# Kernel optimization log

Measured on AMD Instinct MI355X. Metric: run time of the kernel, lower is better.

## Reference

```python
import jax, jax.numpy as jnp
import numpy as np

N_NODES = 50000
N_EDGES = 640000
IN_FEAT = 128
H_FEAT = 128
OUT_FEAT = 128
N_CLASSES = 16
BN_EPS = 1e-5


def gcn_conv(x, W, b, edge_index, n_nodes):
    """PyG GCNConv: add self-loops, symmetric deg^{-1/2} normalization,
    gather -> weighted message -> scatter_add, plus bias."""
    loop = jnp.arange(n_nodes, dtype=edge_index.dtype)
    src = jnp.concatenate([edge_index[0], loop])  # [E+N]
    dst = jnp.concatenate([edge_index[1], loop])  # [E+N]
    ones = jnp.ones(src.shape[0], dtype=x.dtype)
    deg = jax.ops.segment_sum(ones, dst, num_segments=n_nodes)  # >=1 (self loops)
    dinv = jax.lax.rsqrt(deg)
    norm = dinv[src] * dinv[dst]  # [E+N]
    h = x @ W  # [N, F_out]
    msgs = h[src] * norm[:, None]  # gather + scale, [E+N, F_out]
    out = jax.ops.segment_sum(msgs, dst, num_segments=n_nodes)  # scatter_add
    return out + b


def setup_inputs() -> dict:
    key = jax.random.key(0)
    ks = jax.random.split(key, 10)
    seq = jax.random.normal(ks[0], (N_NODES, IN_FEAT), dtype=jnp.float32)
    edge_index = jax.random.randint(ks[1], (2, N_EDGES), 0, N_NODES, dtype=jnp.int64)
    s1 = 1.0 / np.sqrt(IN_FEAT)
    s2 = 1.0 / np.sqrt(H_FEAT)
    s3 = 1.0 / np.sqrt(OUT_FEAT)
    W1 = jax.random.uniform(ks[2], (IN_FEAT, H_FEAT), jnp.float32, -s1, s1)
    b1 = jnp.zeros((H_FEAT,), jnp.float32)
    gamma = jnp.ones((H_FEAT,), jnp.float32)
    beta = jnp.zeros((H_FEAT,), jnp.float32)
    running_mean = 0.1 * jax.random.normal(ks[3], (H_FEAT,), jnp.float32)
    running_var = jax.random.uniform(ks[4], (H_FEAT,), jnp.float32, 0.5, 1.5)
    W2 = jax.random.uniform(ks[5], (H_FEAT, OUT_FEAT), jnp.float32, -s2, s2)
    b2 = jnp.zeros((OUT_FEAT,), jnp.float32)
    Wc = jax.random.uniform(ks[6], (OUT_FEAT, N_CLASSES), jnp.float32, -s3, s3)
    bc = jax.random.uniform(ks[7], (N_CLASSES,), jnp.float32, -s3, s3)
    return {
        "seq": seq, "edge_index": edge_index,
        "W1": W1, "b1": b1, "gamma": gamma, "beta": beta,
        "running_mean": running_mean, "running_var": running_var,
        "W2": W2, "b2": b2, "Wc": Wc, "bc": bc,
    }


def reference(seq, edge_index, W1, b1, gamma, beta, running_mean, running_var, W2, b2, Wc, bc):
    # inference mode: BN uses running stats, dropout is identity
    n = seq.shape[0]
    h = gcn_conv(seq, W1, b1, edge_index, n)
    h = (h - running_mean) * jax.lax.rsqrt(running_var + BN_EPS) * gamma + beta
    h = jax.nn.relu(h)
    h = gcn_conv(h, W2, b2, edge_index, n)
    return h @ Wc + bc
```

## Files before the change

kernel.cpp:

```cpp
#include <hip/hip_runtime.h>
#include <math.h>

#define N_NODES 50000
#define N_EDGES 640000
#define FDIM 128
#define NCLS 16
#define BN_EPS 1e-5f
#define NBS 196
#define NBG 782

typedef __attribute__((ext_vector_type(8))) short bf16x8;
typedef __attribute__((ext_vector_type(4))) float f32x4;

__device__ __forceinline__ unsigned pack_bf16x2(float lo, float hi) {
    unsigned ul = __float_as_uint(lo);
    unsigned uh = __float_as_uint(hi);
    ul += 0x7fff + ((ul >> 16) & 1);
    uh += 0x7fff + ((uh >> 16) & 1);
    return (ul >> 16) | (uh & 0xffff0000u);
}
__device__ __forceinline__ unsigned short bf16_rne(float x) {
    unsigned u = __float_as_uint(x);
    u += 0x7fff + ((u >> 16) & 1);
    return (unsigned short)(u >> 16);
}
__device__ __forceinline__ float bf_lo(unsigned u) { return __uint_as_float(u << 16); }
__device__ __forceinline__ float bf_hi(unsigned u) { return __uint_as_float(u & 0xffff0000u); }

__global__ __launch_bounds__(256) void gemm_count_fold_kernel(
        const float* __restrict__ seq, const float* __restrict__ W1,
        unsigned* __restrict__ bufA,
        const int* __restrict__ eidx, int* __restrict__ deg,
        const float* __restrict__ W2, const float* __restrict__ Wc,
        const float* __restrict__ b1, const float* __restrict__ b2,
        const float* __restrict__ bc, const float* __restrict__ gamma,
        const float* __restrict__ beta, const float* __restrict__ rmean,
        const float* __restrict__ rvar,
        float* __restrict__ W2c, float* __restrict__ bc2, float4* __restrict__ fusedq) {
    __shared__ __align__(16) char smem[65536];
    int tid = threadIdx.x;
    int bid = blockIdx.x;

    if (bid < NBG) {
        bf16x8* WH = (bf16x8*)smem;
        bf16x8* WL = (bf16x8*)(smem + 32768);
        {
            int f0 = tid * 8;
#pragma unroll
            for (int fo = 0; fo < 8; fo++) {
                int fi = f0 + fo;
                int lane = fi & 63, kt = (fi >> 6) & 3, ct = fi >> 8;
                int kbase = kt * 32 + (lane >> 4) * 8;
                int col = ct * 16 + (lane & 15);
                short h[8], lo[8];
#pragma unroll
                for (int j = 0; j < 8; j++) {
                    float wv = W1[(kbase + j) * 128 + col];
                    unsigned short hs = bf16_rne(wv);
                    float rem = wv - __uint_as_float(((unsigned)hs) << 16);
                    h[j] = (short)hs;
                    lo[j] = (short)bf16_rne(rem);
                }
                WH[fi] = *(bf16x8*)h;
                WL[fi] = *(bf16x8*)lo;
            }
        }
        __syncthreads();

        int w = tid >> 6, l = tid & 63;
        int la = l & 15, q = l >> 4;
        int r0 = bid * 64;
        int arow = r0 + w * 16 + la;
        bool rowok = arow < N_NODES;
        const float4* X4 = (const float4*)seq;

        float4 xr[8];
#pragma unroll
        for (int kt = 0; kt < 4; kt++) {
            float4 z4 = make_float4(0.f, 0.f, 0.f, 0.f);
            xr[kt * 2]     = rowok ? X4[arow * 32 + kt * 8 + q * 2]     : z4;
            xr[kt * 2 + 1] = rowok ? X4[arow * 32 + kt * 8 + q * 2 + 1] : z4;
        }
        bf16x8 ah[4], al[4];
#pragma unroll
        for (int kt = 0; kt < 4; kt++) {
            const float* xv = (const float*)&xr[kt * 2];
#pragma unroll
            for (int j = 0; j < 8; j++) {
                float v = xv[j];
                unsigned short hs = bf16_rne(v);
                float rem = v - __uint_as_float(((unsigned)hs) << 16);
                ah[kt][j] = (short)hs;
                al[kt][j] = (short)bf16_rne(rem);
            }
        }
        f32x4 acc[8];
#pragma unroll
        for (int ct = 0; ct < 8; ct++) acc[ct] = (f32x4){0.f, 0.f, 0.f, 0.f};

#pragma unroll
        for (int kt = 0; kt < 4; kt++) {
#pragma unroll
            for (int ct = 0; ct < 8; ct++) {
                bf16x8 bh = WH[(ct * 4 + kt) * 64 + l];
                bf16x8 bl = WL[(ct * 4 + kt) * 64 + l];
                acc[ct] = __builtin_amdgcn_mfma_f32_16x16x32_bf16(ah[kt], bh, acc[ct], 0, 0, 0);
                acc[ct] = __builtin_amdgcn_mfma_f32_16x16x32_bf16(ah[kt], bl, acc[ct], 0, 0, 0);
                acc[ct] = __builtin_amdgcn_mfma_f32_16x16x32_bf16(al[kt], bh, acc[ct], 0, 0, 0);
            }
        }
        __syncthreads();

        float* sC = (float*)smem;
#pragma unroll
        for (int ct = 0; ct < 8; ct++)
#pragma unroll
            for (int r = 0; r < 4; r++)
                sC[(w * 16 + q * 4 + r) * 132 + ct * 16 + la] = acc[ct][r];
        __syncthreads();

        int trow = tid >> 2, tcb = (tid & 3) * 32;
        int grow = r0 + trow;
        if (grow < N_NODES) {
            const float* sr = sC + trow * 132 + tcb;
            unsigned ob[16];
#pragma unroll
            for (int t = 0; t < 16; t++) ob[t] = pack_bf16x2(sr[2 * t], sr[2 * t + 1]);
            uint4* dp = (uint4*)(bufA + (size_t)grow * 64 + (tid & 3) * 16);
#pragma unroll
            for (int g = 0; g < 4; g++)
                dp[g] = make_uint4(ob[g * 4], ob[g * 4 + 1], ob[g * 4 + 2], ob[g * 4 + 3]);
        }
    } else if (bid < NBG + 625) {
        const int4* dst4 = (const int4*)(eidx + N_EDGES);
        int t = (bid - NBG) * 256 + tid;
        int4 d = dst4[t];
        atomicAdd(&deg[d.x], 1);
        atomicAdd(&deg[d.y], 1);
        atomicAdd(&deg[d.z], 1);
        atomicAdd(&deg[d.w], 1);
    } else {
        int fb = bid - (NBG + 625);
        int gid = fb * 256 + tid;
        int r = gid >> 4, c = gid & 15;
        float acc = 0.f;
#pragma unroll 8
        for (int k = 0; k < 128; k++) acc += W2[r * 128 + k] * Wc[k * 16 + c];
        W2c[gid] = acc;
        if (fb == 0) {
            if (tid < 16) {
                float a = bc[tid];
                for (int k = 0; k < 128; k++) a += b2[k] * Wc[k * 16 + tid];
                bc2[tid] = a;
            }
            if (tid < 64) {
                int c0 = tid * 2, c1 = c0 + 1;
                float sc0 = gamma[c0] * rsqrtf(rvar[c0] + BN_EPS);
                float sc1 = gamma[c1] * rsqrtf(rvar[c1] + BN_EPS);
                float sh0 = (b1[c0] - rmean[c0]) * sc0 + beta[c0];
                float sh1 = (b1[c1] - rmean[c1]) * sc1 + beta[c1];
                fusedq[tid] = make_float4(sc0, sh0, sc1, sh1);
            }
        }
    }
}

__global__ __launch_bounds__(256) void scan_kernel(const int* __restrict__ deg,
                                                   int* __restrict__ offs,
                                                   int* __restrict__ partials,
                                                   float* __restrict__ dinv,
                                                   int* __restrict__ cursor,
                                                   int* __restrict__ done) {
    __shared__ int s[256];
    __shared__ int isLast;
    int tid = threadIdx.x;
    int gid = blockIdx.x * 256 + tid;
    int v = (gid < N_NODES) ? deg[gid] : 0;
    if (gid < N_NODES) {
        dinv[gid] = rsqrtf((float)(v + 1));
        cursor[gid] = 0;
    }
    s[tid] = v;
    __syncthreads();
    for (int off = 1; off < 256; off <<= 1) {
        int t2 = (tid >= off) ? s[tid - off] : 0;
        __syncthreads();
        s[tid] += t2;
        __syncthreads();
    }
    if (gid <= N_NODES) offs[gid] = s[tid] - v;
    if (tid == 255) partials[blockIdx.x] = s[255];

    __threadfence();
    if (tid == 0) isLast = (atomicAdd(done, 1) == NBS - 1);
    __syncthreads();
    if (isLast) {
        __threadfence();
        int pv = (tid < NBS) ? partials[tid] : 0;
        s[tid] = pv;
        __syncthreads();
        for (int off = 1; off < 256; off <<= 1) {
            int t2 = (tid >= off) ? s[tid - off] : 0;
            __syncthreads();
            s[tid] += t2;
            __syncthreads();
        }
        if (tid < NBS) partials[tid] = s[tid] - pv;
    }
}

__global__ __launch_bounds__(256) void fill_csr_kernel(const int* __restrict__ eidx,
                                                       const int* __restrict__ offs,
                                                       const int* __restrict__ part,
                                                       const float* __restrict__ dinv,
                                                       int* __restrict__ cursor,
                                                       int2* __restrict__ csr_sw) {
    const int4* src4 = (const int4*)eidx;
    const int4* dst4 = (const int4*)(eidx + N_EDGES);
    int t = blockIdx.x * 256 + threadIdx.x;
    int4 sv = src4[t];
    int4 dv = dst4[t];
    {
        int pos = offs[dv.x] + part[dv.x >> 8] + atomicAdd(&cursor[dv.x], 1);
        csr_sw[pos] = make_int2(sv.x, __float_as_int(dinv[sv.x]));
    }
    {
        int pos = offs[dv.y] + part[dv.y >> 8] + atomicAdd(&cursor[dv.y], 1);
        csr_sw[pos] = make_int2(sv.y, __float_as_int(dinv[sv.y]));
    }
    {
        int pos = offs[dv.z] + part[dv.z >> 8] + atomicAdd(&cursor[dv.z], 1);
        csr_sw[pos] = make_int2(sv.z, __float_as_int(dinv[sv.z]));
    }
    {
        int pos = offs[dv.w] + part[dv.w >> 8] + atomicAdd(&cursor[dv.w], 1);
        csr_sw[pos] = make_int2(sv.w, __float_as_int(dinv[sv.w]));
    }
}

__global__ __launch_bounds__(256) void agg1_kernel(const unsigned* __restrict__ Hb,
                                                   const int2* __restrict__ csr_sw,
                                                   const int* __restrict__ offs,
                                                   const int* __restrict__ part,
                                                   const float* __restrict__ dinv,
                                                   const float4* __restrict__ fusedq,
                                                   const float* __restrict__ W2c,
                                                   float* __restrict__ Z) {
    __shared__ float sH[4][128];
    int w = threadIdx.x >> 6, l = threadIdx.x & 63;
    int node = blockIdx.x * 4 + w;
    int beg = __builtin_amdgcn_readfirstlane(offs[node] + part[node >> 8]);
    int end = __builtin_amdgcn_readfirstlane(offs[node + 1] + part[(node + 1) >> 8]);
    float di = dinv[node];

    int c = l & 15, q = l >> 4;
    float wreg[32];
#pragma unroll
    for (int i = 0; i < 32; i++) wreg[i] = W2c[(q * 32 + i) * 16 + c];

    unsigned hv = Hb[(size_t)node * 64 + l];
    float n2 = di * di;
    float acc0 = bf_lo(hv) * n2, acc1 = bf_hi(hv) * n2;

    int e = beg;
    for (; e + 8 <= end; e += 8) {
        int2 a0 = csr_sw[e];     int2 a1 = csr_sw[e + 1];
        int2 a2 = csr_sw[e + 2]; int2 a3 = csr_sw[e + 3];
        int2 a4 = csr_sw[e + 4]; int2 a5 = csr_sw[e + 5];
        int2 a6 = csr_sw[e + 6]; int2 a7 = csr_sw[e + 7];
        unsigned u0 = Hb[(size_t)a0.x * 64 + l];
        unsigned u1 = Hb[(size_t)a1.x * 64 + l];
        unsigned u2 = Hb[(size_t)a2.x * 64 + l];
        unsigned u3 = Hb[(size_t)a3.x * 64 + l];
        unsigned u4 = Hb[(size_t)a4.x * 64 + l];
        unsigned u5 = Hb[(size_t)a5.x * 64 + l];
        unsigned u6 = Hb[(size_t)a6.x * 64 + l];
        unsigned u7 = Hb[(size_t)a7.x * 64 + l];
        float w0 = __int_as_float(a0.y) * di, w1 = __int_as_float(a1.y) * di;
        float w2 = __int_as_float(a2.y) * di, w3 = __int_as_float(a3.y) * di;
        float w4 = __int_as_float(a4.y) * di, w5 = __int_as_float(a5.y) * di;
        float w6 = __int_as_float(a6.y) * di, w7 = __int_as_float(a7.y) * di;
        acc0 += bf_lo(u0) * w0 + bf_lo(u1) * w1 + bf_lo(u2) * w2 + bf_lo(u3) * w3
              + bf_lo(u4) * w4 + bf_lo(u5) * w5 + bf_lo(u6) * w6 + bf_lo(u7) * w7;
        acc1 += bf_hi(u0) * w0 + bf_hi(u1) * w1 + bf_hi(u2) * w2 + bf_hi(u3) * w3
              + bf_hi(u4) * w4 + bf_hi(u5) * w5 + bf_hi(u6) * w6 + bf_hi(u7) * w7;
    }
    while (e < end) {
        int i1 = e + 1 < end ? e + 1 : end - 1;
        int i2 = e + 2 < end ? e + 2 : end - 1;
        int i3 = e + 3 < end ? e + 3 : end - 1;
        int2 a0 = csr_sw[e];  int2 a1 = csr_sw[i1];
        int2 a2 = csr_sw[i2]; int2 a3 = csr_sw[i3];
        unsigned u0 = Hb[(size_t)a0.x * 64 + l];
        unsigned u1 = Hb[(size_t)a1.x * 64 + l];
        unsigned u2 = Hb[(size_t)a2.x * 64 + l];
        unsigned u3 = Hb[(size_t)a3.x * 64 + l];
        float w0 = __int_as_float(a0.y) * di;
        float w1 = (e + 1 < end) ? __int_as_float(a1.y) * di : 0.f;
        float w2 = (e + 2 < end) ? __int_as_float(a2.y) * di : 0.f;
        float w3 = (e + 3 < end) ? __int_as_float(a3.y) * di : 0.f;
        acc0 += bf_lo(u0) * w0 + bf_lo(u1) * w1 + bf_lo(u2) * w2 + bf_lo(u3) * w3;
        acc1 += bf_hi(u0) * w0 + bf_hi(u1) * w1 + bf_hi(u2) * w2 + bf_hi(u3) * w3;
        e += 4;
    }

    float4 qv = fusedq[l];
    float a0 = fmaxf(acc0 * qv.x + qv.y, 0.f);
    float a1 = fmaxf(acc1 * qv.z + qv.w, 0.f);

    ((float2*)sH[w])[l] = make_float2(a0, a1);
    float z = 0.f;
    const float4* row4 = (const float4*)&sH[w][q * 32];
#pragma unroll
    for (int i = 0; i < 8; i++) {
        float4 v = row4[i];
        z += v.x * wreg[i * 4] + v.y * wreg[i * 4 + 1]
           + v.z * wreg[i * 4 + 2] + v.w * wreg[i * 4 + 3];
    }
    z += __shfl_xor(z, 16);
    z += __shfl_xor(z, 32);
    if (l < 16) Z[(size_t)node * NCLS + l] = z;
}

__global__ __launch_bounds__(256) void agg2_kernel(const float* __restrict__ Z,
                                                   const int2* __restrict__ csr_sw,
                                                   const int* __restrict__ offs,
                                                   const int* __restrict__ part,
                                                   const float* __restrict__ dinv,
                                                   const float* __restrict__ bc2,
                                                   float* __restrict__ out) {
    int grp = threadIdx.x >> 4, c = threadIdx.x & 15;
    int node = blockIdx.x * 16 + grp;
    int beg = offs[node] + part[node >> 8];
    int end = offs[node + 1] + part[(node + 1) >> 8];
    float di = dinv[node];

    float acc = Z[(size_t)node * NCLS + c] * di * di;
    int e = beg;
    for (; e + 8 <= end; e += 8) {
        int2 a0 = csr_sw[e],     a1 = csr_sw[e + 1];
        int2 a2 = csr_sw[e + 2], a3 = csr_sw[e + 3];
        int2 a4 = csr_sw[e + 4], a5 = csr_sw[e + 5];
        int2 a6 = csr_sw[e + 6], a7 = csr_sw[e + 7];
        float v0 = Z[(size_t)a0.x * NCLS + c];
        float v1 = Z[(size_t)a1.x * NCLS + c];
        float v2 = Z[(size_t)a2.x * NCLS + c];
        float v3 = Z[(size_t)a3.x * NCLS + c];
        float v4 = Z[(size_t)a4.x * NCLS + c];
        float v5 = Z[(size_t)a5.x * NCLS + c];
        float v6 = Z[(size_t)a6.x * NCLS + c];
        float v7 = Z[(size_t)a7.x * NCLS + c];
        acc += v0 * (__int_as_float(a0.y) * di) + v1 * (__int_as_float(a1.y) * di)
             + v2 * (__int_as_float(a2.y) * di) + v3 * (__int_as_float(a3.y) * di)
             + v4 * (__int_as_float(a4.y) * di) + v5 * (__int_as_float(a5.y) * di)
             + v6 * (__int_as_float(a6.y) * di) + v7 * (__int_as_float(a7.y) * di);
    }
    for (; e < end; e++) {
        int2 a = csr_sw[e];
        acc += Z[(size_t)a.x * NCLS + c] * (__int_as_float(a.y) * di);
    }
    out[(size_t)node * NCLS + c] = acc + bc2[c];
}

extern "C" void kernel_launch(void* const* d_in, const int* in_sizes, int n_in,
                              void* d_out, int out_size, void* d_ws, size_t ws_size,
                              hipStream_t stream) {
    const float* seq   = (const float*)d_in[0];
    const int*   eidx  = (const int*)d_in[1];
    const float* W1    = (const float*)d_in[2];
    const float* b1    = (const float*)d_in[3];
    const float* gamma = (const float*)d_in[4];
    const float* beta  = (const float*)d_in[5];
    const float* rmean = (const float*)d_in[6];
    const float* rvar  = (const float*)d_in[7];
    const float* W2    = (const float*)d_in[8];
    const float* b2    = (const float*)d_in[9];
    const float* Wc    = (const float*)d_in[10];
    const float* bc    = (const float*)d_in[11];

    char* ws = (char*)d_ws;
    size_t off = 0;
    auto alloc = [&](size_t bytes) -> void* {
        void* p = ws + off;
        off = (off + bytes + 255) & ~(size_t)255;
        return p;
    };
    int*    ctl      = (int*)alloc(256);
    int*    deg      = (int*)alloc(N_NODES * 4);
    int*    cursor   = (int*)alloc(N_NODES * 4);
    int*    offs     = (int*)alloc((N_NODES + 1) * 4);
    int*    partials = (int*)alloc(256 * 4);
    float*  dinv     = (float*)alloc(N_NODES * 4);
    int2*   csr_sw   = (int2*)alloc((size_t)N_EDGES * 8);
    float*  W2c      = (float*)alloc(FDIM * NCLS * 4);
    float*  bc2      = (float*)alloc(NCLS * 4);
    float4* fusedq   = (float4*)alloc(64 * 16);
    unsigned* bufA   = (unsigned*)alloc((size_t)N_NODES * (FDIM / 2) * 4);
    float*  Zbuf     = (float*)alloc((size_t)N_NODES * NCLS * 4);

    hipMemsetAsync(ctl, 0, 256 + (size_t)N_NODES * 4, stream);
    gemm_count_fold_kernel<<<NBG + 625 + 8, 256, 0, stream>>>(
        seq, W1, bufA, eidx, deg, W2, Wc, b1, b2, bc, gamma, beta, rmean, rvar,
        W2c, bc2, fusedq);
    scan_kernel<<<NBS, 256, 0, stream>>>(deg, offs, partials, dinv, cursor, ctl);
    fill_csr_kernel<<<625, 256, 0, stream>>>(eidx, offs, partials, dinv, cursor, csr_sw);
    agg1_kernel<<<N_NODES / 4, 256, 0, stream>>>(bufA, csr_sw, offs, partials,
                                                 dinv, fusedq, W2c, Zbuf);
    agg2_kernel<<<N_NODES / 16, 256, 0, stream>>>(Zbuf, csr_sw, offs, partials,
                                                  dinv, bc2, (float*)d_out);
}
```

Before: 229.2 us.

## Pre-pack W1 split-bf16 fragments once in a separate kernel, read from global in GEMM

Before, each of the 782 GEMM blocks rebuilt the full hi/lo bf16 split of W1 in 64KB of shared memory. That work now happens once in a small 16-block kernel that writes the fragments to global memory, and the GEMM blocks read B fragments straight from global/L2. The GEMM kernel's shared memory shrinks to the 33KB output staging tile, which could allow more resident blocks, and the staging readback is vectorised to float4. The cost is an extra kernel launch and serialisation, plus MFMA operands now coming from L2 instead of LDS.

Measured after the change: 234.4 us. +2.3%, slower.

```diff
diff --git a/kernel.cpp b/kernel.cpp
--- a/kernel.cpp
+++ b/kernel.cpp
@@ -27,127 +27,25 @@
 __device__ __forceinline__ float bf_lo(unsigned u) { return __uint_as_float(u << 16); }
 __device__ __forceinline__ float bf_hi(unsigned u) { return __uint_as_float(u & 0xffff0000u); }
 
-__global__ __launch_bounds__(256) void gemm_count_fold_kernel(
-        const float* __restrict__ seq, const float* __restrict__ W1,
-        unsigned* __restrict__ bufA,
-        const int* __restrict__ eidx, int* __restrict__ deg,
+__global__ __launch_bounds__(256) void packw_fold_kernel(
+        const float* __restrict__ W1,
         const float* __restrict__ W2, const float* __restrict__ Wc,
         const float* __restrict__ b1, const float* __restrict__ b2,
         const float* __restrict__ bc, const float* __restrict__ gamma,
         const float* __restrict__ beta, const float* __restrict__ rmean,
         const float* __restrict__ rvar,
+        bf16x8* __restrict__ WHg, bf16x8* __restrict__ WLg,
         float* __restrict__ W2c, float* __restrict__ bc2, float4* __restrict__ fusedq) {
-    __shared__ __align__(16) char smem[65536];
     int tid = threadIdx.x;
     int bid = blockIdx.x;
-
-    if (bid < NBG) {
-        bf16x8* WH = (bf16x8*)smem;
-        bf16x8* WL = (bf16x8*)(smem + 32768);
-        {
-            int f0 = tid * 8;
-#pragma unroll
-            for (int fo = 0; fo < 8; fo++) {
-                int fi = f0 + fo;
-                int lane = fi & 63, kt = (fi >> 6) & 3, ct = fi >> 8;
-                int kbase = kt * 32 + (lane >> 4) * 8;
-                int col = ct * 16 + (lane & 15);
-                short h[8], lo[8];
-#pragma unroll
-                for (int j = 0; j < 8; j++) {
-                    float wv = W1[(kbase + j) * 128 + col];
-                    unsigned short hs = bf16_rne(wv);
-                    float rem = wv - __uint_as_float(((unsigned)hs) << 16);
-                    h[j] = (short)hs;
-                    lo[j] = (short)bf16_rne(rem);
-                }
-                WH[fi] = *(bf16x8*)h;
-                WL[fi] = *(bf16x8*)lo;
-            }
-        }
-        __syncthreads();
-
-        int w = tid >> 6, l = tid & 63;
-        int la = l & 15, q = l >> 4;
-        int r0 = bid * 64;
-        int arow = r0 + w * 16 + la;
-        bool rowok = arow < N_NODES;
-        const float4* X4 = (const float4*)seq;
-
-        float4 xr[8];
-#pragma unroll
-        for (int kt = 0; kt < 4; kt++) {
-            float4 z4 = make_float4(0.f, 0.f, 0.f, 0.f);
-            xr[kt * 2]     = rowok ? X4[arow * 32 + kt * 8 + q * 2]     : z4;
-            xr[kt * 2 + 1] = rowok ? X4[arow * 32 + kt * 8 + q * 2 + 1] : z4;
-        }
-        bf16x8 ah[4], al[4];
-#pragma unroll
-        for (int kt = 0; kt < 4; kt++) {
-            const float* xv = (const float*)&xr[kt * 2];
-#pragma unroll
-            for (int j = 0; j < 8; j++) {
-                float v = xv[j];
-                unsigned short hs = bf16_rne(v);
-                float rem = v - __uint_as_float(((unsigned)hs) << 16);
-                ah[kt][j] = (short)hs;
-                al[kt][j] = (short)bf16_rne(rem);
-            }
-        }
-        f32x4 acc[8];
-#pragma unroll
-        for (int ct = 0; ct < 8; ct++) acc[ct] = (f32x4){0.f, 0.f, 0.f, 0.f};
-
-#pragma unroll
-        for (int kt = 0; kt < 4; kt++) {
-#pragma unroll
-            for (int ct = 0; ct < 8; ct++) {
-                bf16x8 bh = WH[(ct * 4 + kt) * 64 + l];
-                bf16x8 bl = WL[(ct * 4 + kt) * 64 + l];
-                acc[ct] = __builtin_amdgcn_mfma_f32_16x16x32_bf16(ah[kt], bh, acc[ct], 0, 0, 0);
-                acc[ct] = __builtin_amdgcn_mfma_f32_16x16x32_bf16(ah[kt], bl, acc[ct], 0, 0, 0);
-                acc[ct] = __builtin_amdgcn_mfma_f32_16x16x32_bf16(al[kt], bh, acc[ct], 0, 0, 0);
-            }
-        }
-        __syncthreads();
-
-        float* sC = (float*)smem;
-#pragma unroll
-        for (int ct = 0; ct < 8; ct++)
-#pragma unroll
-            for (int r = 0; r < 4; r++)
-                sC[(w * 16 + q * 4 + r) * 132 + ct * 16 + la] = acc[ct][r];
-        __syncthreads();
-
-        int trow = tid >> 2, tcb = (tid & 3) * 32;
-        int grow = r0 + trow;
-        if (grow < N_NODES) {
-            const float* sr = sC + trow * 132 + tcb;
-            unsigned ob[16];
-#pragma unroll
-            for (int t = 0; t < 16; t++) ob[t] = pack_bf16x2(sr[2 * t], sr[2 * t + 1]);
-            uint4* dp = (uint4*)(bufA + (size_t)grow * 64 + (tid & 3) * 16);
-#pragma unroll
-            for (int g = 0; g < 4; g++)
-                dp[g] = make_uint4(ob[g * 4], ob[g * 4 + 1], ob[g * 4 + 2], ob[g * 4 + 3]);
-        }
-    } else if (bid < NBG + 625) {
-        const int4* dst4 = (const int4*)(eidx + N_EDGES);
-        int t = (bid - NBG) * 256 + tid;
-        int4 d = dst4[t];
-        atomicAdd(&deg[d.x], 1);
-        atomicAdd(&deg[d.y], 1);
-        atomicAdd(&deg[d.z], 1);
-        atomicAdd(&deg[d.w], 1);
-    } else {
-        int fb = bid - (NBG + 625);
-        int gid = fb * 256 + tid;
+    if (bid < 8) {
+        int gid = bid * 256 + tid;
         int r = gid >> 4, c = gid & 15;
         float acc = 0.f;
 #pragma unroll 8
         for (int k = 0; k < 128; k++) acc += W2[r * 128 + k] * Wc[k * 16 + c];
         W2c[gid] = acc;
-        if (fb == 0) {
+        if (bid == 0) {
             if (tid < 16) {
                 float a = bc[tid];
                 for (int k = 0; k < 128; k++) a += b2[k] * Wc[k * 16 + tid];
@@ -162,6 +60,109 @@
                 fusedq[tid] = make_float4(sc0, sh0, sc1, sh1);
             }
         }
+    } else {
+        int fi = (bid - 8) * 256 + tid;
+        int lane = fi & 63, kt = (fi >> 6) & 3, ct = fi >> 8;
+        int kbase = kt * 32 + (lane >> 4) * 8;
+        int col = ct * 16 + (lane & 15);
+        short h[8], lo[8];
+#pragma unroll
+        for (int j = 0; j < 8; j++) {
+            float wv = W1[(kbase + j) * 128 + col];
+            unsigned short hs = bf16_rne(wv);
+            float rem = wv - __uint_as_float(((unsigned)hs) << 16);
+            h[j] = (short)hs;
+            lo[j] = (short)bf16_rne(rem);
+        }
+        WHg[fi] = *(bf16x8*)h;
+        WLg[fi] = *(bf16x8*)lo;
+    }
+}
+
+__global__ __launch_bounds__(256) void gemm_count_kernel(
+        const float* __restrict__ seq,
+        const bf16x8* __restrict__ WHg, const bf16x8* __restrict__ WLg,
+        unsigned* __restrict__ bufA,
+        const int* __restrict__ eidx, int* __restrict__ deg) {
+    __shared__ __align__(16) float sC[64 * 132];
+    int tid = threadIdx.x;
+    int bid = blockIdx.x;
+
+    if (bid < NBG) {
+        int w = tid >> 6, l = tid & 63;
+        int la = l & 15, q = l >> 4;
+        int r0 = bid * 64;
+        int arow = r0 + w * 16 + la;
+        bool rowok = arow < N_NODES;
+        const float4* X4 = (const float4*)seq;
+
+        float4 xr[8];
+#pragma unroll
+        for (int kt = 0; kt < 4; kt++) {
+            float4 z4 = make_float4(0.f, 0.f, 0.f, 0.f);
+            xr[kt * 2]     = rowok ? X4[arow * 32 + kt * 8 + q * 2]     : z4;
+            xr[kt * 2 + 1] = rowok ? X4[arow * 32 + kt * 8 + q * 2 + 1] : z4;
+        }
+        bf16x8 ah[4], al[4];
+#pragma unroll
+        for (int kt = 0; kt < 4; kt++) {
+            const float* xv = (const float*)&xr[kt * 2];
+#pragma unroll
+            for (int j = 0; j < 8; j++) {
+                float v = xv[j];
+                unsigned short hs = bf16_rne(v);
+                float rem = v - __uint_as_float(((unsigned)hs) << 16);
+                ah[kt][j] = (short)hs;
+                al[kt][j] = (short)bf16_rne(rem);
+            }
+        }
+        f32x4 acc[8];
+#pragma unroll
+        for (int ct = 0; ct < 8; ct++) acc[ct] = (f32x4){0.f, 0.f, 0.f, 0.f};
+
+#pragma unroll
+        for (int kt = 0; kt < 4; kt++) {
+#pragma unroll
+            for (int ct = 0; ct < 8; ct++) {
+                bf16x8 bh = WHg[(ct * 4 + kt) * 64 + l];
+                bf16x8 bl = WLg[(ct * 4 + kt) * 64 + l];
+                acc[ct] = __builtin_amdgcn_mfma_f32_16x16x32_bf16(ah[kt], bh, acc[ct], 0, 0, 0);
+                acc[ct] = __builtin_amdgcn_mfma_f32_16x16x32_bf16(ah[kt], bl, acc[ct], 0, 0, 0);
+                acc[ct] = __builtin_amdgcn_mfma_f32_16x16x32_bf16(al[kt], bh, acc[ct], 0, 0, 0);
+            }
+        }
+
+#pragma unroll
+        for (int ct = 0; ct < 8; ct++)
+#pragma unroll
+            for (int r = 0; r < 4; r++)
+                sC[(w * 16 + q * 4 + r) * 132 + ct * 16 + la] = acc[ct][r];
+        __syncthreads();
+
+        int trow = tid >> 2, tcb = (tid & 3) * 32;
+        int grow = r0 + trow;
+        if (grow < N_NODES) {
+            const float4* sr4 = (const float4*)(sC + trow * 132 + tcb);
+            unsigned ob[16];
+#pragma unroll
+            for (int t = 0; t < 8; t++) {
+                float4 v = sr4[t];
+                ob[2 * t]     = pack_bf16x2(v.x, v.y);
+                ob[2 * t + 1] = pack_bf16x2(v.z, v.w);
+            }
+            uint4* dp = (uint4*)(bufA + (size_t)grow * 64 + (tid & 3) * 16);
+#pragma unroll
+            for (int g = 0; g < 4; g++)
+                dp[g] = make_uint4(ob[g * 4], ob[g * 4 + 1], ob[g * 4 + 2], ob[g * 4 + 3]);
+        }
+    } else {
+        const int4* dst4 = (const int4*)(eidx + N_EDGES);
+        int t = (bid - NBG) * 256 + tid;
+        int4 d = dst4[t];
+        atomicAdd(&deg[d.x], 1);
+        atomicAdd(&deg[d.y], 1);
+        atomicAdd(&deg[d.z], 1);
+        atomicAdd(&deg[d.w], 1);
     }
 }
 
@@ -395,13 +396,15 @@
     float*  W2c      = (float*)alloc(FDIM * NCLS * 4);
     float*  bc2      = (float*)alloc(NCLS * 4);
     float4* fusedq   = (float4*)alloc(64 * 16);
+    bf16x8* WHg      = (bf16x8*)alloc(2048 * 16);
+    bf16x8* WLg      = (bf16x8*)alloc(2048 * 16);
     unsigned* bufA   = (unsigned*)alloc((size_t)N_NODES * (FDIM / 2) * 4);
     float*  Zbuf     = (float*)alloc((size_t)N_NODES * NCLS * 4);
 
     hipMemsetAsync(ctl, 0, 256 + (size_t)N_NODES * 4, stream);
-    gemm_count_fold_kernel<<<NBG + 625 + 8, 256, 0, stream>>>(
-        seq, W1, bufA, eidx, deg, W2, Wc, b1, b2, bc, gamma, beta, rmean, rvar,
-        W2c, bc2, fusedq);
+    packw_fold_kernel<<<16, 256, 0, stream>>>(W1, W2, Wc, b1, b2, bc, gamma, beta,
+                                              rmean, rvar, WHg, WLg, W2c, bc2, fusedq);
+    gemm_count_kernel<<<NBG + 625, 256, 0, stream>>>(seq, WHg, WLg, bufA, eidx, deg);
     scan_kernel<<<NBS, 256, 0, stream>>>(deg, offs, partials, dinv, cursor, ctl);
     fill_csr_kernel<<<625, 256, 0, stream>>>(eidx, offs, partials, dinv, cursor, csr_sw);
     agg1_kernel<<<N_NODES / 4, 256, 0, stream>>>(bufA, csr_sw, offs, partials,
```
